# Optimization experiments

Hardware: AMD Instinct MI355X
Metric: run time of the kernel (lower is better)

The kernel has to match this reference:

```python
import jax, jax.numpy as jnp
import numpy as np

N = 4_194_304
NUM_ITER = 6
DAMPING = 0.95
TOL = 1e-06
EPS = 1e-12


def _translate_x(dx):
    """4x4 homogeneous translation along the optical (x) axis."""
    return jnp.eye(4, dtype=dx.dtype).at[0, 3].set(dx)


def setup_inputs() -> dict:
    key = jax.random.key(0)
    k1, k2, k3 = jax.random.split(key, 3)
    # Ray origins: near x = -10, transverse spread within/around the aperture
    px = -10.0 + 0.5 * jax.random.normal(k1, (N, 1), dtype=jnp.float32)
    pyz = 8.0 * jax.random.normal(k2, (N, 2), dtype=jnp.float32)
    P = jnp.concatenate([px, pyz], axis=-1)
    # Ray directions: mostly +x, small transverse components, normalized
    vyz = 0.05 * jax.random.normal(k3, (N, 2), dtype=jnp.float32)
    V = jnp.concatenate([jnp.ones((N, 1), jnp.float32), vyz], axis=-1)
    V = V / jnp.linalg.norm(V, axis=-1, keepdims=True)
    tf = jnp.eye(4, dtype=jnp.float32)
    return {
        "P": P,
        "V": V,
        "tf": tf,
        "diameter": jnp.float32(50.0),
        "C": jnp.float32(0.02),
        "anchors": jnp.zeros((2,), jnp.float32),
        "scale": jnp.float32(1.0),
        "normalize": jnp.asarray(False),
    }


def reference(P, V, tf, diameter, C, anchors, scale, normalize):
    # normalize: curvature interpreted relative to semi-diameter
    C_eff = jnp.where(normalize, C * 2.0 / diameter, C)
    s2 = scale * scale

    def sag(r2):  # scaled spherical sag: f = scale * g(r2/scale^2)
        u = r2 / s2
        root = jnp.sqrt(jnp.clip(1.0 - C_eff * C_eff * u, EPS))
        return scale * C_eff * u / (1.0 + root)

    def sag_grad(y, z):  # (df/dy, df/dz) = C*(y,z) / (scale*sqrt(1-C^2 u))
        u = (y * y + z * z) / s2
        root = jnp.sqrt(jnp.clip(1.0 - C_eff * C_eff * u, EPS))
        k = C_eff / (scale * root)
        return k * y, k * z

    # anchors shift the surface along x by fractions of the edge sag (extent)
    extent = sag(jnp.square(diameter * 0.5))
    surface_tf = tf @ _translate_x(-anchors[0] * extent)
    next_tf = tf @ _translate_x((anchors[1] - anchors[0]) * extent)

    # Rays into surface-local frame
    R = surface_tf[:3, :3]
    tv = surface_tf[:3, 3]
    Pl = (P - tv) @ R  # [N,3] = R^T (P - t)
    Vl = V @ R
    vx, vy, vz = Vl[:, 0], Vl[:, 1], Vl[:, 2]

    safe_vx = jnp.where(jnp.abs(vx) > EPS, vx, EPS)
    t = -Pl[:, 0] / safe_vx  # init: intersection with plane x=0

    # Damped Newton on F(t) = sag(y(t),z(t)) - x(t)
    for _ in range(NUM_ITER):
        p = Pl + t[:, None] * Vl
        y, z = p[:, 1], p[:, 2]
        F = sag(y * y + z * z) - p[:, 0]
        gy, gz = sag_grad(y, z)
        dF = gy * vy + gz * vz - vx
        dF = jnp.where(jnp.abs(dF) > EPS, dF, EPS)
        t = t - DAMPING * F / dF

    p = Pl + t[:, None] * Vl
    y, z = p[:, 1], p[:, 2]
    r2 = y * y + z * z
    F = sag(r2) - p[:, 0]
    gy, gz = sag_grad(y, z)
    # implicit-surface normal: grad(sag(y,z) - x) = (-1, gy, gz), normalized
    n_local = jnp.stack([-jnp.ones_like(gy), gy, gz], axis=-1)
    n_local = n_local / jnp.linalg.norm(n_local, axis=-1, keepdims=True)
    normals = n_local @ R.T  # back to global frame

    valid = (r2 <= jnp.square(diameter * 0.5)) & (jnp.abs(F) < 100.0 * TOL)
    return t, normals, valid, surface_tf, next_tf
```

## Files before the change

### kernel.cpp

```cpp
#include <hip/hip_runtime.h>

#define F_EPS 1e-12f
#define F_DAMPING 0.95f
#define N_ITER 6

struct Params {
    float R[9];
    float tv[3];
    float C_eff;
    float s2;
    float scale;
    float half_d2;
    float inv_s2;
};

__global__ void setup_kernel(const float* __restrict__ tf,
                             const float* __restrict__ diameter,
                             const float* __restrict__ C,
                             const float* __restrict__ anchors,
                             const float* __restrict__ scale,
                             const unsigned char* __restrict__ normalize,
                             float* __restrict__ out_tail,
                             Params* __restrict__ params)
{
#pragma clang fp contract(off)
    if (threadIdx.x != 0 || blockIdx.x != 0) return;
    float d  = diameter[0];
    float c  = C[0];
    float sc = scale[0];
    bool  nrm = (normalize[0] != 0);
    float C_eff = nrm ? (c * 2.0f / d) : c;
    float s2 = sc * sc;
    float hr = d * 0.5f;
    float hr2 = hr * hr;
    float u = hr2 / s2;
    float root = sqrtf(fmaxf(1.0f - (C_eff * C_eff) * u, F_EPS));
    float extent = sc * C_eff * u / (1.0f + root);
    float a0 = anchors[0], a1 = anchors[1];
    float dx0 = -a0 * extent;
    float dx1 = (a1 - a0) * extent;
    for (int i = 0; i < 4; ++i) {
        for (int j = 0; j < 4; ++j) {
            float v = tf[i * 4 + j];
            float sv = (j == 3) ? (tf[i * 4 + 0] * dx0 + v) : v;
            float nv = (j == 3) ? (tf[i * 4 + 0] * dx1 + v) : v;
            out_tail[i * 4 + j]      = sv;
            out_tail[16 + i * 4 + j] = nv;
        }
    }
    for (int k = 0; k < 3; ++k) {
        for (int j = 0; j < 3; ++j)
            params->R[k * 3 + j] = tf[k * 4 + j];
        params->tv[k] = tf[k * 4 + 0] * dx0 + tf[k * 4 + 3];
    }
    params->C_eff   = C_eff;
    params->s2      = s2;
    params->scale   = sc;
    params->half_d2 = hr2;
    params->inv_s2  = 1.0f / s2;
}

__launch_bounds__(256)
__global__ void trace_kernel(const float* __restrict__ P,
                             const float* __restrict__ V,
                             const Params* __restrict__ pp,
                             float* __restrict__ out,
                             int n)
{
    int tid = blockIdx.x * blockDim.x + threadIdx.x;
    int base = tid * 4;
    if (base >= n) return;

    float R0 = pp->R[0], R1 = pp->R[1], R2 = pp->R[2];
    float R3 = pp->R[3], R4 = pp->R[4], R5 = pp->R[5];
    float R6 = pp->R[6], R7 = pp->R[7], R8 = pp->R[8];
    float tv0 = pp->tv[0], tv1 = pp->tv[1], tv2 = pp->tv[2];
    float C_eff = pp->C_eff, scale = pp->scale, half_d2 = pp->half_d2;
    float inv_s2 = pp->inv_s2;
    float ce2 = C_eff * C_eff;
    float sC  = scale * C_eff;
    float a_num = sC * inv_s2;
    float ce2s  = ce2 * inv_s2;
    float Cs    = C_eff / scale;

    float Px[4], Py[4], Pz[4], Vx[4], Vy[4], Vz[4];
    if (base + 4 <= n) {
        const float4* P4 = reinterpret_cast<const float4*>(P + (size_t)base * 3);
        const float4* V4 = reinterpret_cast<const float4*>(V + (size_t)base * 3);
        float4 pa = P4[0], pb = P4[1], pc = P4[2];
        float4 va = V4[0], vb = V4[1], vc = V4[2];
        Px[0] = pa.x; Py[0] = pa.y; Pz[0] = pa.z;
        Px[1] = pa.w; Py[1] = pb.x; Pz[1] = pb.y;
        Px[2] = pb.z; Py[2] = pb.w; Pz[2] = pc.x;
        Px[3] = pc.y; Py[3] = pc.z; Pz[3] = pc.w;
        Vx[0] = va.x; Vy[0] = va.y; Vz[0] = va.z;
        Vx[1] = va.w; Vy[1] = vb.x; Vz[1] = vb.y;
        Vx[2] = vb.z; Vy[2] = vb.w; Vz[2] = vc.x;
        Vx[3] = vc.y; Vy[3] = vc.z; Vz[3] = vc.w;
    } else {
        for (int r = 0; r < 4; ++r) {
            int i = base + r;
            if (i < n) {
                Px[r] = P[(size_t)i * 3 + 0]; Py[r] = P[(size_t)i * 3 + 1]; Pz[r] = P[(size_t)i * 3 + 2];
                Vx[r] = V[(size_t)i * 3 + 0]; Vy[r] = V[(size_t)i * 3 + 1]; Vz[r] = V[(size_t)i * 3 + 2];
            } else {
                Px[r] = 0.0f; Py[r] = 0.0f; Pz[r] = 0.0f;
                Vx[r] = 1.0f; Vy[r] = 0.0f; Vz[r] = 0.0f;
            }
        }
    }

    float Plx[4], Ply[4], Plz[4], vx[4], vy[4], vz[4], t[4];
#pragma unroll
    for (int r = 0; r < 4; ++r) {
        float px0 = Px[r] - tv0, py0 = Py[r] - tv1, pz0 = Pz[r] - tv2;
        Plx[r] = px0 * R0 + py0 * R3 + pz0 * R6;
        Ply[r] = px0 * R1 + py0 * R4 + pz0 * R7;
        Plz[r] = px0 * R2 + py0 * R5 + pz0 * R8;
        vx[r] = Vx[r] * R0 + Vy[r] * R3 + Vz[r] * R6;
        vy[r] = Vx[r] * R1 + Vy[r] * R4 + Vz[r] * R7;
        vz[r] = Vx[r] * R2 + Vy[r] * R5 + Vz[r] * R8;
        float safe_vx = (fabsf(vx[r]) > F_EPS) ? vx[r] : F_EPS;
        t[r] = (-Plx[r]) * __builtin_amdgcn_rcpf(safe_vx);
    }

#pragma unroll
    for (int it = 0; it < N_ITER; ++it) {
#pragma unroll
        for (int r = 0; r < 4; ++r) {
            float pxx = fmaf(t[r], vx[r], Plx[r]);
            float py  = fmaf(t[r], vy[r], Ply[r]);
            float pz  = fmaf(t[r], vz[r], Plz[r]);
            float r2  = fmaf(py, py, pz * pz);
            float m   = fmaxf(fmaf(-ce2s, r2, 1.0f), F_EPS);
            float rsq = __builtin_amdgcn_rsqf(m);
            float root = m * rsq;
            float k    = Cs * rsq;
            float ird  = __builtin_amdgcn_rcpf(1.0f + root);
            float F    = fmaf(a_num * r2, ird, -pxx);
            float dF = fmaf(k * py, vy[r], fmaf(k * pz, vz[r], -vx[r]));
            dF = (fabsf(dF) > F_EPS) ? dF : F_EPS;
            t[r] = fmaf(-F_DAMPING * F, __builtin_amdgcn_rcpf(dF), t[r]);
        }
    }

    float tres[4], nxo[4], nyo[4], nzo[4], val[4];
#pragma unroll
    for (int r = 0; r < 4; ++r) {
        float pxx = fmaf(t[r], vx[r], Plx[r]);
        float py  = fmaf(t[r], vy[r], Ply[r]);
        float pz  = fmaf(t[r], vz[r], Plz[r]);
        float r2  = fmaf(py, py, pz * pz);
        float m   = fmaxf(fmaf(-ce2s, r2, 1.0f), F_EPS);
        float rsq = __builtin_amdgcn_rsqf(m);
        float root = m * rsq;
        float k    = Cs * rsq;
        float ird  = __builtin_amdgcn_rcpf(1.0f + root);
        float F    = fmaf(a_num * r2, ird, -pxx);
        float gy = k * py, gz = k * pz;
        float nn2 = fmaf(gy, gy, fmaf(gz, gz, 1.0f));
        float irn = __builtin_amdgcn_rsqf(nn2);
        float nlx = -irn, nly = gy * irn, nlz = gz * irn;
        nxo[r] = nlx * R0 + nly * R1 + nlz * R2;
        nyo[r] = nlx * R3 + nly * R4 + nlz * R5;
        nzo[r] = nlx * R6 + nly * R7 + nlz * R8;
        tres[r] = t[r];
        val[r]  = ((r2 <= half_d2) && (fabsf(F) < 1e-4f)) ? 1.0f : 0.0f;
    }

    float* t_out = out;
    float* n_out = out + (size_t)n;
    float* v_out = out + (size_t)n * 4;
    if (base + 4 <= n) {
        *reinterpret_cast<float4*>(t_out + base) = make_float4(tres[0], tres[1], tres[2], tres[3]);
        float4* N4 = reinterpret_cast<float4*>(n_out + (size_t)base * 3);
        N4[0] = make_float4(nxo[0], nyo[0], nzo[0], nxo[1]);
        N4[1] = make_float4(nyo[1], nzo[1], nxo[2], nyo[2]);
        N4[2] = make_float4(nzo[2], nxo[3], nyo[3], nzo[3]);
        *reinterpret_cast<float4*>(v_out + base) = make_float4(val[0], val[1], val[2], val[3]);
    } else {
        for (int r = 0; r < 4; ++r) {
            int i = base + r;
            if (i < n) {
                t_out[i] = tres[r];
                n_out[(size_t)i * 3 + 0] = nxo[r];
                n_out[(size_t)i * 3 + 1] = nyo[r];
                n_out[(size_t)i * 3 + 2] = nzo[r];
                v_out[i] = val[r];
            }
        }
    }
}

extern "C" void kernel_launch(void* const* d_in, const int* in_sizes, int n_in,
                              void* d_out, int out_size, void* d_ws, size_t ws_size,
                              hipStream_t stream) {
    const float* P  = (const float*)d_in[0];
    const float* V  = (const float*)d_in[1];
    const float* tf = (const float*)d_in[2];
    const float* diameter = (const float*)d_in[3];
    const float* C  = (const float*)d_in[4];
    const float* anchors = (const float*)d_in[5];
    const float* scale = (const float*)d_in[6];
    const unsigned char* normalize = (const unsigned char*)d_in[7];
    int n = in_sizes[0] / 3;
    float* out = (float*)d_out;
    float* out_tail = out + (size_t)n * 5;
    Params* params = (Params*)d_ws;

    setup_kernel<<<1, 1, 0, stream>>>(tf, diameter, C, anchors, scale, normalize,
                                      out_tail, params);
    int threads = 256;
    int nthreads = (n + 3) / 4;
    int blocks = (nthreads + threads - 1) / threads;
    trace_kernel<<<blocks, threads, 0, stream>>>(P, V, params, out, n);
}
```

Baseline: 180.5 us.

## Fuse setup into trace kernel and stage AoS loads/stores through LDS

Removes the separate single-thread setup kernel; every thread now recomputes the scalar parameters and block 0 writes the transform outputs. Per-thread strided float4 loads of P/V and stores of normals become fully coalesced block-wide float4 accesses, transposed through shared memory. This saves a launch and its dependency gap and improves memory coalescing. In exchange it adds LDS traffic, several barriers and redundant scalar math in every thread.

```diff
diff --git a/kernel.cpp b/kernel.cpp
--- a/kernel.cpp
+++ b/kernel.cpp
@@ -3,106 +3,93 @@
 #define F_EPS 1e-12f
 #define F_DAMPING 0.95f
 #define N_ITER 6
-
-struct Params {
-    float R[9];
-    float tv[3];
-    float C_eff;
-    float s2;
-    float scale;
-    float half_d2;
-    float inv_s2;
-};
-
-__global__ void setup_kernel(const float* __restrict__ tf,
-                             const float* __restrict__ diameter,
-                             const float* __restrict__ C,
-                             const float* __restrict__ anchors,
-                             const float* __restrict__ scale,
-                             const unsigned char* __restrict__ normalize,
-                             float* __restrict__ out_tail,
-                             Params* __restrict__ params)
-{
-#pragma clang fp contract(off)
-    if (threadIdx.x != 0 || blockIdx.x != 0) return;
-    float d  = diameter[0];
-    float c  = C[0];
-    float sc = scale[0];
-    bool  nrm = (normalize[0] != 0);
-    float C_eff = nrm ? (c * 2.0f / d) : c;
-    float s2 = sc * sc;
-    float hr = d * 0.5f;
-    float hr2 = hr * hr;
-    float u = hr2 / s2;
-    float root = sqrtf(fmaxf(1.0f - (C_eff * C_eff) * u, F_EPS));
-    float extent = sc * C_eff * u / (1.0f + root);
-    float a0 = anchors[0], a1 = anchors[1];
-    float dx0 = -a0 * extent;
-    float dx1 = (a1 - a0) * extent;
-    for (int i = 0; i < 4; ++i) {
-        for (int j = 0; j < 4; ++j) {
-            float v = tf[i * 4 + j];
-            float sv = (j == 3) ? (tf[i * 4 + 0] * dx0 + v) : v;
-            float nv = (j == 3) ? (tf[i * 4 + 0] * dx1 + v) : v;
-            out_tail[i * 4 + j]      = sv;
-            out_tail[16 + i * 4 + j] = nv;
-        }
-    }
-    for (int k = 0; k < 3; ++k) {
-        for (int j = 0; j < 3; ++j)
-            params->R[k * 3 + j] = tf[k * 4 + j];
-        params->tv[k] = tf[k * 4 + 0] * dx0 + tf[k * 4 + 3];
-    }
-    params->C_eff   = C_eff;
-    params->s2      = s2;
-    params->scale   = sc;
-    params->half_d2 = hr2;
-    params->inv_s2  = 1.0f / s2;
-}
-
-__launch_bounds__(256)
+#define TPB 256
+
+__launch_bounds__(TPB)
 __global__ void trace_kernel(const float* __restrict__ P,
                              const float* __restrict__ V,
-                             const Params* __restrict__ pp,
+                             const float* __restrict__ tf,
+                             const float* __restrict__ diameter,
+                             const float* __restrict__ Cc,
+                             const float* __restrict__ anchors,
+                             const float* __restrict__ scale_p,
+                             const unsigned char* __restrict__ normalize,
                              float* __restrict__ out,
                              int n)
 {
-    int tid = blockIdx.x * blockDim.x + threadIdx.x;
-    int base = tid * 4;
-    if (base >= n) return;
-
-    float R0 = pp->R[0], R1 = pp->R[1], R2 = pp->R[2];
-    float R3 = pp->R[3], R4 = pp->R[4], R5 = pp->R[5];
-    float R6 = pp->R[6], R7 = pp->R[7], R8 = pp->R[8];
-    float tv0 = pp->tv[0], tv1 = pp->tv[1], tv2 = pp->tv[2];
-    float C_eff = pp->C_eff, scale = pp->scale, half_d2 = pp->half_d2;
-    float inv_s2 = pp->inv_s2;
-    float ce2 = C_eff * C_eff;
-    float sC  = scale * C_eff;
+    __shared__ float4 sbuf[TPB * 3];
+    const int tid  = threadIdx.x;
+    const int base = (blockIdx.x * TPB + tid) * 4;
+
+    float R0,R1,R2,R3,R4,R5,R6,R7,R8, tv0,tv1,tv2;
+    float C_eff, scale, half_d2, inv_s2;
+    {
+#pragma clang fp contract(off)
+        float d  = diameter[0];
+        float c  = Cc[0];
+        float sc = scale_p[0];
+        bool  nrm = (normalize[0] != 0);
+        C_eff = nrm ? (c * 2.0f / d) : c;
+        float s2 = sc * sc;
+        float hr = d * 0.5f;
+        half_d2 = hr * hr;
+        float u = half_d2 / s2;
+        float root = sqrtf(fmaxf(1.0f - (C_eff * C_eff) * u, F_EPS));
+        float extent = sc * C_eff * u / (1.0f + root);
+        float a0 = anchors[0], a1 = anchors[1];
+        float dx0 = -a0 * extent;
+        float dx1 = (a1 - a0) * extent;
+        R0 = tf[0]; R1 = tf[1]; R2 = tf[2];
+        R3 = tf[4]; R4 = tf[5]; R5 = tf[6];
+        R6 = tf[8]; R7 = tf[9]; R8 = tf[10];
+        tv0 = tf[0] * dx0 + tf[3];
+        tv1 = tf[4] * dx0 + tf[7];
+        tv2 = tf[8] * dx0 + tf[11];
+        scale  = sc;
+        inv_s2 = 1.0f / s2;
+        if (blockIdx.x == 0 && tid < 16) {
+            int i = tid >> 2, j = tid & 3;
+            float v  = tf[tid];
+            float sv = (j == 3) ? (tf[i * 4] * dx0 + v) : v;
+            float nv = (j == 3) ? (tf[i * 4] * dx1 + v) : v;
+            float* out_tail = out + (size_t)n * 5;
+            out_tail[tid]      = sv;
+            out_tail[16 + tid] = nv;
+        }
+    }
+    float ce2   = C_eff * C_eff;
+    float sC    = scale * C_eff;
     float a_num = sC * inv_s2;
     float ce2s  = ce2 * inv_s2;
     float Cs    = C_eff / scale;
 
+    const bool full_block = ((blockIdx.x + 1) * (TPB * 4) <= n);
+
     float Px[4], Py[4], Pz[4], Vx[4], Vy[4], Vz[4];
-    if (base + 4 <= n) {
-        const float4* P4 = reinterpret_cast<const float4*>(P + (size_t)base * 3);
-        const float4* V4 = reinterpret_cast<const float4*>(V + (size_t)base * 3);
-        float4 pa = P4[0], pb = P4[1], pc = P4[2];
-        float4 va = V4[0], vb = V4[1], vc = V4[2];
-        Px[0] = pa.x; Py[0] = pa.y; Pz[0] = pa.z;
-        Px[1] = pa.w; Py[1] = pb.x; Pz[1] = pb.y;
-        Px[2] = pb.z; Py[2] = pb.w; Pz[2] = pc.x;
-        Px[3] = pc.y; Py[3] = pc.z; Pz[3] = pc.w;
-        Vx[0] = va.x; Vy[0] = va.y; Vz[0] = va.z;
-        Vx[1] = va.w; Vy[1] = vb.x; Vz[1] = vb.y;
-        Vx[2] = vb.z; Vy[2] = vb.w; Vz[2] = vc.x;
-        Vx[3] = vc.y; Vy[3] = vc.z; Vz[3] = vc.w;
+    if (full_block) {
+        const size_t bf4 = (size_t)blockIdx.x * (TPB * 3);
+        const float4* P4 = reinterpret_cast<const float4*>(P);
+        const float4* V4 = reinterpret_cast<const float4*>(V);
+        float4 p0 = P4[bf4 + tid], p1 = P4[bf4 + TPB + tid], p2 = P4[bf4 + 2*TPB + tid];
+        float4 q0 = V4[bf4 + tid], q1 = V4[bf4 + TPB + tid], q2 = V4[bf4 + 2*TPB + tid];
+        sbuf[tid] = p0; sbuf[TPB + tid] = p1; sbuf[2*TPB + tid] = p2;
+        __syncthreads();
+        float4 a = sbuf[3*tid], b = sbuf[3*tid + 1], c = sbuf[3*tid + 2];
+        __syncthreads();
+        Px[0]=a.x; Py[0]=a.y; Pz[0]=a.z; Px[1]=a.w; Py[1]=b.x; Pz[1]=b.y;
+        Px[2]=b.z; Py[2]=b.w; Pz[2]=c.x; Px[3]=c.y; Py[3]=c.z; Pz[3]=c.w;
+        sbuf[tid] = q0; sbuf[TPB + tid] = q1; sbuf[2*TPB + tid] = q2;
+        __syncthreads();
+        a = sbuf[3*tid]; b = sbuf[3*tid + 1]; c = sbuf[3*tid + 2];
+        __syncthreads();
+        Vx[0]=a.x; Vy[0]=a.y; Vz[0]=a.z; Vx[1]=a.w; Vy[1]=b.x; Vz[1]=b.y;
+        Vx[2]=b.z; Vy[2]=b.w; Vz[2]=c.x; Vx[3]=c.y; Vy[3]=c.z; Vz[3]=c.w;
     } else {
         for (int r = 0; r < 4; ++r) {
             int i = base + r;
             if (i < n) {
-                Px[r] = P[(size_t)i * 3 + 0]; Py[r] = P[(size_t)i * 3 + 1]; Pz[r] = P[(size_t)i * 3 + 2];
-                Vx[r] = V[(size_t)i * 3 + 0]; Vy[r] = V[(size_t)i * 3 + 1]; Vz[r] = V[(size_t)i * 3 + 2];
+                Px[r] = P[(size_t)i*3 + 0]; Py[r] = P[(size_t)i*3 + 1]; Pz[r] = P[(size_t)i*3 + 2];
+                Vx[r] = V[(size_t)i*3 + 0]; Vy[r] = V[(size_t)i*3 + 1]; Vz[r] = V[(size_t)i*3 + 2];
             } else {
                 Px[r] = 0.0f; Py[r] = 0.0f; Pz[r] = 0.0f;
                 Vx[r] = 1.0f; Vy[r] = 0.0f; Vz[r] = 0.0f;
@@ -110,7 +97,7 @@
         }
     }
 
-    float Plx[4], Ply[4], Plz[4], vx[4], vy[4], vz[4], t[4];
+    float Plx[4], Ply[4], Plz[4], vx[4], vy[4], vz[4], tN[4];
 #pragma unroll
     for (int r = 0; r < 4; ++r) {
         float px0 = Px[r] - tv0, py0 = Py[r] - tv1, pz0 = Pz[r] - tv2;
@@ -121,16 +108,16 @@
         vy[r] = Vx[r] * R1 + Vy[r] * R4 + Vz[r] * R7;
         vz[r] = Vx[r] * R2 + Vy[r] * R5 + Vz[r] * R8;
         float safe_vx = (fabsf(vx[r]) > F_EPS) ? vx[r] : F_EPS;
-        t[r] = (-Plx[r]) * __builtin_amdgcn_rcpf(safe_vx);
+        tN[r] = (-Plx[r]) * __builtin_amdgcn_rcpf(safe_vx);
     }
 
 #pragma unroll
     for (int it = 0; it < N_ITER; ++it) {
 #pragma unroll
         for (int r = 0; r < 4; ++r) {
-            float pxx = fmaf(t[r], vx[r], Plx[r]);
-            float py  = fmaf(t[r], vy[r], Ply[r]);
-            float pz  = fmaf(t[r], vz[r], Plz[r]);
+            float pxx = fmaf(tN[r], vx[r], Plx[r]);
+            float py  = fmaf(tN[r], vy[r], Ply[r]);
+            float pz  = fmaf(tN[r], vz[r], Plz[r]);
             float r2  = fmaf(py, py, pz * pz);
             float m   = fmaxf(fmaf(-ce2s, r2, 1.0f), F_EPS);
             float rsq = __builtin_amdgcn_rsqf(m);
@@ -140,16 +127,16 @@
             float F    = fmaf(a_num * r2, ird, -pxx);
             float dF = fmaf(k * py, vy[r], fmaf(k * pz, vz[r], -vx[r]));
             dF = (fabsf(dF) > F_EPS) ? dF : F_EPS;
-            t[r] = fmaf(-F_DAMPING * F, __builtin_amdgcn_rcpf(dF), t[r]);
+            tN[r] = fmaf(-F_DAMPING * F, __builtin_amdgcn_rcpf(dF), tN[r]);
         }
     }
 
     float tres[4], nxo[4], nyo[4], nzo[4], val[4];
 #pragma unroll
     for (int r = 0; r < 4; ++r) {
-        float pxx = fmaf(t[r], vx[r], Plx[r]);
-        float py  = fmaf(t[r], vy[r], Ply[r]);
-        float pz  = fmaf(t[r], vz[r], Plz[r]);
+        float pxx = fmaf(tN[r], vx[r], Plx[r]);
+        float py  = fmaf(tN[r], vy[r], Ply[r]);
+        float pz  = fmaf(tN[r], vz[r], Plz[r]);
         float r2  = fmaf(py, py, pz * pz);
         float m   = fmaxf(fmaf(-ce2s, r2, 1.0f), F_EPS);
         float rsq = __builtin_amdgcn_rsqf(m);
@@ -164,28 +151,33 @@
         nxo[r] = nlx * R0 + nly * R1 + nlz * R2;
         nyo[r] = nlx * R3 + nly * R4 + nlz * R5;
         nzo[r] = nlx * R6 + nly * R7 + nlz * R8;
-        tres[r] = t[r];
+        tres[r] = tN[r];
         val[r]  = ((r2 <= half_d2) && (fabsf(F) < 1e-4f)) ? 1.0f : 0.0f;
     }
 
     float* t_out = out;
     float* n_out = out + (size_t)n;
     float* v_out = out + (size_t)n * 4;
-    if (base + 4 <= n) {
+    if (full_block) {
+        sbuf[3*tid]     = make_float4(nxo[0], nyo[0], nzo[0], nxo[1]);
+        sbuf[3*tid + 1] = make_float4(nyo[1], nzo[1], nxo[2], nyo[2]);
+        sbuf[3*tid + 2] = make_float4(nzo[2], nxo[3], nyo[3], nzo[3]);
+        __syncthreads();
+        const size_t bf4 = (size_t)blockIdx.x * (TPB * 3);
+        float4* N4 = reinterpret_cast<float4*>(n_out);
+        N4[bf4 + tid]         = sbuf[tid];
+        N4[bf4 + TPB + tid]   = sbuf[TPB + tid];
+        N4[bf4 + 2*TPB + tid] = sbuf[2*TPB + tid];
         *reinterpret_cast<float4*>(t_out + base) = make_float4(tres[0], tres[1], tres[2], tres[3]);
-        float4* N4 = reinterpret_cast<float4*>(n_out + (size_t)base * 3);
-        N4[0] = make_float4(nxo[0], nyo[0], nzo[0], nxo[1]);
-        N4[1] = make_float4(nyo[1], nzo[1], nxo[2], nyo[2]);
-        N4[2] = make_float4(nzo[2], nxo[3], nyo[3], nzo[3]);
         *reinterpret_cast<float4*>(v_out + base) = make_float4(val[0], val[1], val[2], val[3]);
     } else {
         for (int r = 0; r < 4; ++r) {
             int i = base + r;
             if (i < n) {
                 t_out[i] = tres[r];
-                n_out[(size_t)i * 3 + 0] = nxo[r];
-                n_out[(size_t)i * 3 + 1] = nyo[r];
-                n_out[(size_t)i * 3 + 2] = nzo[r];
+                n_out[(size_t)i*3 + 0] = nxo[r];
+                n_out[(size_t)i*3 + 1] = nyo[r];
+                n_out[(size_t)i*3 + 2] = nzo[r];
                 v_out[i] = val[r];
             }
         }
@@ -205,13 +197,9 @@
     const unsigned char* normalize = (const unsigned char*)d_in[7];
     int n = in_sizes[0] / 3;
     float* out = (float*)d_out;
-    float* out_tail = out + (size_t)n * 5;
-    Params* params = (Params*)d_ws;
-
-    setup_kernel<<<1, 1, 0, stream>>>(tf, diameter, C, anchors, scale, normalize,
-                                      out_tail, params);
-    int threads = 256;
-    int nthreads = (n + 3) / 4;
-    int blocks = (nthreads + threads - 1) / threads;
-    trace_kernel<<<blocks, threads, 0, stream>>>(P, V, params, out, n);
+
+    int rays_per_block = TPB * 4;
+    int blocks = (n + rays_per_block - 1) / rays_per_block;
+    trace_kernel<<<blocks, TPB, 0, stream>>>(P, V, tf, diameter, C, anchors, scale,
+                                             normalize, out, n);
 }
```

Result: no change. 177.1 us (-1.9%).
